# Kernel tuning notes

Hardware: AMD Instinct MI355X
Metric: run time of the kernel (lower is better)

Reference implementation:

```python
import jax, jax.numpy as jnp
import numpy as np

TEMPERATURE = 0.07
MARGIN = 0.2
SHUF_ID_OFFSET = 100000


def _normalize(x):
    # matches F.normalize(x + 1e-8, dim=-1) with default eps=1e-12
    v = x + 1e-8
    n = jnp.linalg.norm(v, axis=-1, keepdims=True)
    return v / jnp.maximum(n, 1e-12)


def setup_inputs() -> dict:
    key = jax.random.key(0)
    k1, k2, k3, k4 = jax.random.split(key, 4)
    M, C, D = 1024, 3, 512
    return {
        "motion_embs": jax.random.normal(k1, (M, D), dtype=jnp.float32),
        "text_embs": jax.random.normal(k2, (M, C, D), dtype=jnp.float32),
        "shuffled_text_embs": jax.random.normal(k3, (M, C, D), dtype=jnp.float32),
        "motion_ids": jax.random.randint(k4, (M,), 0, 256, dtype=jnp.int64 if jax.config.jax_enable_x64 else jnp.int32),
    }


def reference(motion_embs, text_embs, shuffled_text_embs, motion_ids):
    M, C, D = text_embs.shape
    m = _normalize(motion_embs)                       # [M, D]
    t = _normalize(text_embs).reshape(M * C, D)       # [M*C, D]
    s = _normalize(shuffled_text_embs).reshape(M * C, D)

    emb = jnp.concatenate([m, t, s], axis=0)          # [N, D], N = M + 2*M*C
    ids = jnp.concatenate([
        motion_ids,
        jnp.repeat(motion_ids, C),
        jnp.repeat(motion_ids + SHUF_ID_OFFSET, C),
    ])

    sim = (emb @ emb.T) / TEMPERATURE                 # [N, N]
    N = emb.shape[0]
    same = ids[None, :] == ids[:, None]
    eye = jnp.eye(N, dtype=bool)
    pos_mask = same & ~eye
    neg_mask = (~same) & ~eye

    exp_sim = jnp.exp(sim)
    # denominator over positives + negatives (all off-diagonal), as in the original
    denom = jnp.sum(jnp.where(pos_mask | neg_mask, exp_sim, 0.0), axis=1)   # [N]
    n_pos = jnp.sum(pos_mask, axis=1)
    n_neg = jnp.sum(neg_mask, axis=1)

    pos_sum = jnp.sum(jnp.where(pos_mask, sim, 0.0), axis=1)
    infonce = jnp.log(denom) - pos_sum / jnp.maximum(n_pos, 1)               # [N]

    margin = jnp.sum(jnp.where(neg_mask, jnp.maximum(sim + MARGIN, 0.0), 0.0), axis=1) / jnp.maximum(n_neg, 1)

    valid = (n_pos > 0) & (n_neg > 0)
    count = jnp.sum(valid)
    total = jnp.sum(jnp.where(valid, infonce + margin, 0.0))
    loss = jnp.where(count > 0, total / jnp.maximum(count, 1), 0.0)
    return loss
```

## Files before the change

### kernel.cpp

```cpp
#include <hip/hip_runtime.h>

#define M_ROWS 1024
#define DIM 512
#define NB 1024
#define N_TOT 7168
#define TEXT_OFF 1024
#define SHUF_OFF 4096
#define INV_T (1.0f/0.07f)
#define MARGIN_V 0.2f
#define TILES2 28
#define NBLK2 406
#define SLOT 1536

typedef __attribute__((ext_vector_type(8))) short bf16x8;
typedef __attribute__((ext_vector_type(4))) float f32x4;

typedef const __attribute__((address_space(1))) unsigned int gas_uint;
typedef __attribute__((address_space(3))) unsigned int las_uint;

__device__ __forceinline__ void gload16(const void* g, void* l) {
  __builtin_amdgcn_global_load_lds((gas_uint*)g, (las_uint*)l, 16, 0, 0);
}

__device__ __forceinline__ ushort f2bf(float f) {
  unsigned u = __float_as_uint(f);
  u += 0x7fffu + ((u >> 16) & 1u);
  return (ushort)(u >> 16);
}

__global__ __launch_bounds__(256) void k_normalize(
    const float* __restrict__ motion, const float* __restrict__ text,
    const float* __restrict__ shuf, const int* __restrict__ mids,
    ushort* __restrict__ emb, int* __restrict__ ids) {
  int wave = threadIdx.x >> 6;
  int lane = threadIdx.x & 63;
  int row = blockIdx.x * 4 + wave;
  if (row >= N_TOT) return;
  const float* src;
  int id;
  if (row < TEXT_OFF) { src = motion + (size_t)row * DIM; id = mids[row]; }
  else if (row < SHUF_OFF) { int r = row - TEXT_OFF; src = text + (size_t)r * DIM; id = mids[r / 3]; }
  else { int r = row - SHUF_OFF; src = shuf + (size_t)r * DIM; id = mids[r / 3] + 100000; }

  float4 a = ((const float4*)src)[lane * 2];
  float4 b = ((const float4*)src)[lane * 2 + 1];
  float v0 = a.x + 1e-8f, v1 = a.y + 1e-8f, v2 = a.z + 1e-8f, v3 = a.w + 1e-8f;
  float v4 = b.x + 1e-8f, v5 = b.y + 1e-8f, v6 = b.z + 1e-8f, v7 = b.w + 1e-8f;
  float ss = v0*v0 + v1*v1 + v2*v2 + v3*v3 + v4*v4 + v5*v5 + v6*v6 + v7*v7;
  #pragma unroll
  for (int m = 1; m < 64; m <<= 1) ss += __shfl_xor(ss, m);
  float inv = 1.0f / fmaxf(sqrtf(ss), 1e-12f);

  uint w0 = (uint)f2bf(v0 * inv) | ((uint)f2bf(v1 * inv) << 16);
  uint w1 = (uint)f2bf(v2 * inv) | ((uint)f2bf(v3 * inv) << 16);
  uint w2 = (uint)f2bf(v4 * inv) | ((uint)f2bf(v5 * inv) << 16);
  uint w3 = (uint)f2bf(v6 * inv) | ((uint)f2bf(v7 * inv) << 16);
  uint4 pk; pk.x = w0; pk.y = w1; pk.z = w2; pk.w = w3;
  *((uint4*)(emb + (size_t)row * DIM + lane * 8)) = pk;
  if (lane == 0) ids[row] = id;
}

__global__ __launch_bounds__(512, 2) void k_gemm_loss(
    const ushort* __restrict__ emb, const int* __restrict__ ids,
    float* __restrict__ part) {
  __shared__ ushort Asm[3][8192];
  __shared__ ushort Bsm[3][8192];

  int orig = blockIdx.x;
  int xcd = orig & 7;
  int idx = orig >> 3;
  int bid = (xcd < 6 ? xcd * 51 : 306 + (xcd - 6) * 50) + idx;

  int x = 0;
  while (bid >= TILES2 - x) { bid -= TILES2 - x; x++; }
  int y = x + bid;
  bool diag = (x == y);
  int brow = x * 256, bcol = y * 256;
  int tbid = x * TILES2 - x * (x - 1) / 2 + (y - x);

  int t = threadIdx.x;
  int l = t & 63;
  int w = t >> 6;
  int wr = w >> 2;
  int wc = w & 3;
  int fr = l & 15;
  int fg = l >> 4;

  int srow = w * 16 + (l >> 2);
  int scol = ((l & 3) ^ ((l >> 3) & 3)) * 16;
  const char* gA = (const char*)emb + (size_t)(brow + srow) * NB + scol;
  const char* gB = (const char*)emb + (size_t)(bcol + srow) * NB + scol;
  int ldso = w * 512;

  f32x4 acc[8][4];
  #pragma unroll
  for (int m = 0; m < 8; m++)
    #pragma unroll
    for (int n = 0; n < 4; n++)
      acc[m][n] = (f32x4){0.f, 0.f, 0.f, 0.f};

  int swz = (fg ^ ((fr >> 1) & 3)) * 8;

#define STAGE(T) do { \
    const int _b = (T) % 3; const int _kb = (T) * 64; \
    gload16(gA + _kb,          &Asm[_b][ldso]); \
    gload16(gA + 131072 + _kb, &Asm[_b][4096 + ldso]); \
    gload16(gB + _kb,          &Bsm[_b][ldso]); \
    gload16(gB + 131072 + _kb, &Bsm[_b][4096 + ldso]); \
  } while (0)

  STAGE(0);
  STAGE(1);
  asm volatile("s_waitcnt vmcnt(4)" ::: "memory");
  __builtin_amdgcn_s_barrier();

  #pragma unroll
  for (int tt = 0; tt < 16; tt++) {
    if (tt + 2 < 16) STAGE(tt + 2);
    const int _b = tt % 3;
    const ushort* Ab = &Asm[_b][(wr * 128 + fr) * 32 + swz];
    const ushort* Bb = &Bsm[_b][(wc * 64 + fr) * 32 + swz];
    bf16x8 aF[8], bF[4];
    #pragma unroll
    for (int m = 0; m < 8; m++) aF[m] = *(const bf16x8*)(Ab + m * 512);
    #pragma unroll
    for (int n = 0; n < 4; n++) bF[n] = *(const bf16x8*)(Bb + n * 512);
    __builtin_amdgcn_s_setprio(1);
    #pragma unroll
    for (int m = 0; m < 8; m++)
      #pragma unroll
      for (int n = 0; n < 4; n++)
        acc[m][n] = __builtin_amdgcn_mfma_f32_16x16x32_bf16(aF[m], bF[n], acc[m][n], 0, 0, 0);
    __builtin_amdgcn_s_setprio(0);
    if (tt < 14) {
      asm volatile("s_waitcnt vmcnt(4)" ::: "memory");
      __builtin_amdgcn_s_barrier();
    } else if (tt == 14) {
      asm volatile("s_waitcnt vmcnt(0)" ::: "memory");
      __builtin_amdgcn_s_barrier();
    }
  }
#undef STAGE

  __syncthreads();
  float* rpd = (float*)&Asm[0][0];
  float* rpp = rpd + 1024;
  float* rpm = rpp + 1024;
  float* cps = (float*)&Bsm[0][0];
  int* ridL = (int*)&Bsm[1][0];
  int* cidL = ridL + 256;
  if (t < 256) ridL[t] = ids[brow + t];
  else cidL[t - 256] = ids[bcol + (t - 256)];
  __syncthreads();

  float* ps = part + (size_t)tbid * SLOT;

  int cl = fr;
  int cgrp = fg;
  int cidv[4];
  #pragma unroll
  for (int n = 0; n < 4; n++) cidv[n] = cidL[wc * 64 + n * 16 + cl];
  float cd[4], cp[4], cm[4];
  #pragma unroll
  for (int n = 0; n < 4; n++) { cd[n] = 0.f; cp[n] = 0.f; cm[n] = 0.f; }

  #pragma unroll
  for (int m = 0; m < 8; m++) {
    #pragma unroll
    for (int r = 0; r < 4; r++) {
      int row_l = wr * 128 + m * 16 + cgrp * 4 + r;
      int i = brow + row_l;
      int idi = ridL[row_l];
      float dsum = 0.f, psum = 0.f, msum = 0.f;
      #pragma unroll
      for (int n = 0; n < 4; n++) {
        int col_l = wc * 64 + n * 16 + cl;
        int j = bcol + col_l;
        float sim = acc[m][n][r] * INV_T;
        bool live = (!diag) || (i != j);
        if (live) {
          float e = __expf(sim);
          float hinge = fmaxf(sim + MARGIN_V, 0.f);
          bool same = (idi == cidv[n]);
          float psv = same ? sim : 0.f;
          float msv = same ? 0.f : hinge;
          dsum += e; psum += psv; msum += msv;
          if (!diag) { cd[n] += e; cp[n] += psv; cm[n] += msv; }
        }
      }
      #pragma unroll
      for (int s = 1; s < 16; s <<= 1) {
        dsum += __shfl_xor(dsum, s);
        psum += __shfl_xor(psum, s);
        msum += __shfl_xor(msum, s);
      }
      if (cl == 0) {
        int o = w * 128 + (row_l & 127);
        rpd[o] = dsum; rpp[o] = psum; rpm[o] = msum;
      }
    }
  }

  if (!diag) {
    #pragma unroll
    for (int n = 0; n < 4; n++) {
      float d = cd[n], p = cp[n], mm = cm[n];
      d += __shfl_xor(d, 16); d += __shfl_xor(d, 32);
      p += __shfl_xor(p, 16); p += __shfl_xor(p, 32);
      mm += __shfl_xor(mm, 16); mm += __shfl_xor(mm, 32);
      if (l < 16) {
        int o = ((w * 4 + n) * 16 + cl) * 3;
        cps[o] = d; cps[o + 1] = p; cps[o + 2] = mm;
      }
    }
  }
  __syncthreads();

  if (t < 256) {
    int b0 = (t >> 7) * 512 + (t & 127);
    float d = rpd[b0] + rpd[b0 + 128] + rpd[b0 + 256] + rpd[b0 + 384];
    float p = rpp[b0] + rpp[b0 + 128] + rpp[b0 + 256] + rpp[b0 + 384];
    float mm = rpm[b0] + rpm[b0 + 128] + rpm[b0 + 256] + rpm[b0 + 384];
    ps[t] = d; ps[256 + t] = p; ps[512 + t] = mm;
  }
  if (!diag && wr == 0 && l < 16) {
    #pragma unroll
    for (int n = 0; n < 4; n++) {
      int o0 = ((w * 4 + n) * 16 + cl) * 3;
      int o1 = (((w + 4) * 4 + n) * 16 + cl) * 3;
      int col_l = wc * 64 + n * 16 + cl;
      ps[768 + col_l] = cps[o0] + cps[o1];
      ps[768 + 256 + col_l] = cps[o0 + 1] + cps[o1 + 1];
      ps[768 + 512 + col_l] = cps[o0 + 2] + cps[o1 + 2];
    }
  }
}

__global__ __launch_bounds__(256) void k_reduce(
    const float* __restrict__ part, const int* __restrict__ mids,
    float* __restrict__ blockout) {
  __shared__ int hist[256];
  __shared__ float reds[256];
  __shared__ int redc[256];
  int t = threadIdx.x;
  hist[t] = 0;
  __syncthreads();
  for (int i = t; i < M_ROWS; i += 256) atomicAdd(&hist[mids[i]], 1);
  __syncthreads();

  int p = blockIdx.x;
  int i = p * 256 + t;
  float d = 0.f, pp = 0.f, mm = 0.f;
  int base = p * TILES2 - p * (p - 1) / 2;
  for (int yy = p; yy < TILES2; yy++) {
    const float* s = part + (size_t)(base + yy - p) * SLOT;
    d += s[t]; pp += s[256 + t]; mm += s[512 + t];
  }
  for (int xx = 0; xx < p; xx++) {
    int b = xx * TILES2 - xx * (xx - 1) / 2 + (p - xx);
    const float* s = part + (size_t)b * SLOT + 768;
    d += s[t]; pp += s[256 + t]; mm += s[512 + t];
  }

  int vmid; bool sh = false;
  if (i < TEXT_OFF) vmid = mids[i];
  else if (i < SHUF_OFF) vmid = mids[(i - TEXT_OFF) / 3];
  else { vmid = mids[(i - SHUF_OFF) / 3]; sh = true; }
  int c = hist[vmid];
  int npos = sh ? (3 * c - 1) : (4 * c - 1);
  int nneg = N_TOT - 1 - npos;
  float val = 0.f; int cnt = 0;
  if (npos > 0 && nneg > 0) {
    val = logf(d) - pp / (float)(npos > 1 ? npos : 1) + mm / (float)(nneg > 1 ? nneg : 1);
    cnt = 1;
  }
  reds[t] = val; redc[t] = cnt;
  __syncthreads();
  for (int s2 = 128; s2 > 0; s2 >>= 1) {
    if (t < s2) { reds[t] += reds[t + s2]; redc[t] += redc[t + s2]; }
    __syncthreads();
  }
  if (t == 0) { blockout[p * 2] = reds[0]; blockout[p * 2 + 1] = (float)redc[0]; }
}

__global__ __launch_bounds__(64) void k_final(
    const float* __restrict__ blockout, float* __restrict__ out) {
  int t = threadIdx.x;
  float s = 0.f, c = 0.f;
  if (t < TILES2) { s = blockout[t * 2]; c = blockout[t * 2 + 1]; }
  #pragma unroll
  for (int m = 32; m > 0; m >>= 1) { s += __shfl_down(s, m); c += __shfl_down(c, m); }
  if (t == 0) out[0] = (c > 0.f) ? s / c : 0.f;
}

extern "C" void kernel_launch(void* const* d_in, const int* in_sizes, int n_in,
                              void* d_out, int out_size, void* d_ws, size_t ws_size,
                              hipStream_t stream) {
  const float* motion = (const float*)d_in[0];
  const float* text   = (const float*)d_in[1];
  const float* shuf   = (const float*)d_in[2];
  const int*   mids   = (const int*)d_in[3];

  char* ws = (char*)d_ws;
  ushort* emb = (ushort*)ws;
  int* ids    = (int*)(ws + (size_t)N_TOT * DIM * 2);
  float* blockout = (float*)(ws + 7368704);
  float* part = (float*)(ws + 7454720);

  k_normalize<<<N_TOT / 4, 256, 0, stream>>>(motion, text, shuf, mids, emb, ids);
  k_gemm_loss<<<NBLK2, 512, 0, stream>>>(emb, ids, part);
  k_reduce<<<TILES2, 256, 0, stream>>>(part, mids, blockout);
  k_final<<<1, 64, 0, stream>>>(blockout, (float*)d_out);
}
```

Measured before the change: 81.61 us.

## Load GEMM fragments directly from global memory instead of LDS triple-buffering

Removes the LDS staging pipeline (global_load_lds into triple-buffered, swizzled shared tiles with waitcnt/barrier sync). Each wave now loads its bf16 MFMA fragments directly from global memory. Shared memory shrinks to just the epilogue reduction buffers, and the ids are loaded up front. This removes barriers and LDS traffic. In exchange, each row of A is re-read by 4 waves and each row of B by 2 waves, and global latency is no longer hidden by explicit prefetch, so the loop relies on L1/L2 hits and the compiler's scheduling.

```diff
diff --git a/kernel.cpp b/kernel.cpp
--- a/kernel.cpp
+++ b/kernel.cpp
@@ -14,13 +14,6 @@
 
 typedef __attribute__((ext_vector_type(8))) short bf16x8;
 typedef __attribute__((ext_vector_type(4))) float f32x4;
-
-typedef const __attribute__((address_space(1))) unsigned int gas_uint;
-typedef __attribute__((address_space(3))) unsigned int las_uint;
-
-__device__ __forceinline__ void gload16(const void* g, void* l) {
-  __builtin_amdgcn_global_load_lds((gas_uint*)g, (las_uint*)l, 16, 0, 0);
-}
 
 __device__ __forceinline__ ushort f2bf(float f) {
   unsigned u = __float_as_uint(f);
@@ -63,8 +56,12 @@
 __global__ __launch_bounds__(512, 2) void k_gemm_loss(
     const ushort* __restrict__ emb, const int* __restrict__ ids,
     float* __restrict__ part) {
-  __shared__ ushort Asm[3][8192];
-  __shared__ ushort Bsm[3][8192];
+  __shared__ float rpd[1024];
+  __shared__ float rpp[1024];
+  __shared__ float rpm[1024];
+  __shared__ float cps[1536];
+  __shared__ int ridL[256];
+  __shared__ int cidL[256];
 
   int orig = blockIdx.x;
   int xcd = orig & 7;
@@ -86,11 +83,8 @@
   int fr = l & 15;
   int fg = l >> 4;
 
-  int srow = w * 16 + (l >> 2);
-  int scol = ((l & 3) ^ ((l >> 3) & 3)) * 16;
-  const char* gA = (const char*)emb + (size_t)(brow + srow) * NB + scol;
-  const char* gB = (const char*)emb + (size_t)(bcol + srow) * NB + scol;
-  int ldso = w * 512;
+  if (t < 256) ridL[t] = ids[brow + t];
+  else if (t < 512) cidL[t - 256] = ids[bcol + (t - 256)];
 
   f32x4 acc[8][4];
   #pragma unroll
@@ -99,58 +93,25 @@
     for (int n = 0; n < 4; n++)
       acc[m][n] = (f32x4){0.f, 0.f, 0.f, 0.f};
 
-  int swz = (fg ^ ((fr >> 1) & 3)) * 8;
-
-#define STAGE(T) do { \
-    const int _b = (T) % 3; const int _kb = (T) * 64; \
-    gload16(gA + _kb,          &Asm[_b][ldso]); \
-    gload16(gA + 131072 + _kb, &Asm[_b][4096 + ldso]); \
-    gload16(gB + _kb,          &Bsm[_b][ldso]); \
-    gload16(gB + 131072 + _kb, &Bsm[_b][4096 + ldso]); \
-  } while (0)
-
-  STAGE(0);
-  STAGE(1);
-  asm volatile("s_waitcnt vmcnt(4)" ::: "memory");
-  __builtin_amdgcn_s_barrier();
-
-  #pragma unroll
-  for (int tt = 0; tt < 16; tt++) {
-    if (tt + 2 < 16) STAGE(tt + 2);
-    const int _b = tt % 3;
-    const ushort* Ab = &Asm[_b][(wr * 128 + fr) * 32 + swz];
-    const ushort* Bb = &Bsm[_b][(wc * 64 + fr) * 32 + swz];
+  const char* pa = (const char*)emb + (size_t)(brow + wr * 128 + fr) * NB + fg * 16;
+  const char* pb = (const char*)emb + (size_t)(bcol + wc * 64 + fr) * NB + fg * 16;
+
+  #pragma unroll
+  for (int kk = 0; kk < 16; kk++) {
     bf16x8 aF[8], bF[4];
     #pragma unroll
-    for (int m = 0; m < 8; m++) aF[m] = *(const bf16x8*)(Ab + m * 512);
-    #pragma unroll
-    for (int n = 0; n < 4; n++) bF[n] = *(const bf16x8*)(Bb + n * 512);
-    __builtin_amdgcn_s_setprio(1);
+    for (int m = 0; m < 8; m++)
+      aF[m] = *(const bf16x8*)(pa + (size_t)m * 16 * NB + kk * 64);
+    #pragma unroll
+    for (int n = 0; n < 4; n++)
+      bF[n] = *(const bf16x8*)(pb + (size_t)n * 16 * NB + kk * 64);
     #pragma unroll
     for (int m = 0; m < 8; m++)
       #pragma unroll
       for (int n = 0; n < 4; n++)
         acc[m][n] = __builtin_amdgcn_mfma_f32_16x16x32_bf16(aF[m], bF[n], acc[m][n], 0, 0, 0);
-    __builtin_amdgcn_s_setprio(0);
-    if (tt < 14) {
-      asm volatile("s_waitcnt vmcnt(4)" ::: "memory");
-      __builtin_amdgcn_s_barrier();
-    } else if (tt == 14) {
-      asm volatile("s_waitcnt vmcnt(0)" ::: "memory");
-      __builtin_amdgcn_s_barrier();
-    }
-  }
-#undef STAGE
-
-  __syncthreads();
-  float* rpd = (float*)&Asm[0][0];
-  float* rpp = rpd + 1024;
-  float* rpm = rpp + 1024;
-  float* cps = (float*)&Bsm[0][0];
-  int* ridL = (int*)&Bsm[1][0];
-  int* cidL = ridL + 256;
-  if (t < 256) ridL[t] = ids[brow + t];
-  else cidL[t - 256] = ids[bcol + (t - 256)];
+  }
+
   __syncthreads();
 
   float* ps = part + (size_t)tbid * SLOT;
```

Result: slower. 140.3 us (+72.0%).
